# Kernel optimization log

Hardware: AMD Instinct MI355X
Metric: run time of the kernel (lower is better)

Reference implementation:

```python
import jax, jax.numpy as jnp
import numpy as np

P_MASK = 0.2
HALF = (2, 25, 25)            # n_consecutive // 2 for (T, H, W)
NPIX = 5 * 51 * 51            # np.prod(n_consecutive) = 13005


def setup_inputs() -> dict:
    key = jax.random.key(0)
    ks = jax.random.split(key, 10)
    B, T, H, W, C = 4, 32, 224, 224, 3
    N = 2000
    frames = jax.random.normal(ks[0], (B, T, H, W, C), dtype=jnp.float32)
    mask_token = jax.random.normal(ks[1], (C,), dtype=jnp.float32)
    b = jax.random.randint(ks[2], (N,), 0, B)
    t = jax.random.randint(ks[3], (N,), 0, T)
    h = jax.random.randint(ks[4], (N,), 0, H)
    w = jax.random.randint(ks[5], (N,), 0, W)
    rb = jax.random.randint(ks[6], (1,), 0, B)
    rt = jax.random.randint(ks[7], (1,), 0, T)
    rh = jax.random.randint(ks[8], (1,), 0, H)
    rw = jax.random.randint(ks[9], (1,), 0, W)
    return dict(frames=frames, mask_token=mask_token, b=b, t=t, h=h, w=w,
                rb=rb, rt=rt, rh=rh, rw=rw)


def _axis_mask(idx, half, size):
    # [n_box, size] float indicator of max(0, idx-half) <= pos < min(idx+half, size-1)
    lo = jnp.maximum(idx - half, 0)[:, None]
    hi = jnp.minimum(idx + half, size - 1)[:, None]   # torch slice upper bound uses size-1
    pos = jnp.arange(size)[None, :]
    return ((pos >= lo) & (pos < hi)).astype(jnp.float32)


def _box_union(b, t, h, w, B, T, H, W):
    # union of all boxes as a single rank-1-factor contraction (no per-box scatter)
    bi = (jnp.arange(B)[None, :] == b[:, None]).astype(jnp.float32)
    ti = _axis_mask(t, HALF[0], T)
    hi = _axis_mask(h, HALF[1], H)
    wi = _axis_mask(w, HALF[2], W)
    return jnp.einsum('ib,it,ih,iw->bthw', bi, ti, hi, wi) > 0


def reference(frames, mask_token, b, t, h, w, rb, rt, rh, rw):
    B, T, H, W, C = frames.shape
    tnpix = B * T * H * W
    n1 = int(tnpix * P_MASK * 0.8 // NPIX)
    n2 = int(tnpix * P_MASK * 0.1 // NPIX)
    R1 = _box_union(b[:n1], t[:n1], h[:n1], w[:n1], B, T, H, W)
    R2 = _box_union(b[n1:n1 + n2], t[n1:n1 + n2], h[n1:n1 + n2], w[n1:n1 + n2], B, T, H, W)
    R3 = _box_union(b[n1 + n2:n1 + 2 * n2], t[n1 + n2:n1 + 2 * n2],
                    h[n1 + n2:n1 + 2 * n2], w[n1 + n2:n1 + 2 * n2], B, T, H, W)
    random_token = frames[rb[0], rt[0], rh[0], rw[0]]   # [C]
    out = jnp.where(R1[..., None], mask_token, frames)
    out = jnp.where(R2[..., None], random_token, out)
    M = (R1 | R2 | R3).reshape(B, T, -1).any(axis=-1)
    return out, M
```

## Files before the change

### kernel.cpp

```cpp
#include <hip/hip_runtime.h>

namespace {
constexpr int B_ = 4, T_ = 32, H_ = 224, W_ = 224;
constexpr int HW_ = H_ * W_;
constexpr int NPIX_ = B_ * T_ * HW_;
constexpr int N1_ = 79;
constexpr int N2_ = 9;
constexpr int NBOX_RW_ = N1_ + N2_;
constexpr int NBOX_M_  = N1_ + 2 * N2_;
constexpr int HALF_T = 2, HALF_HW = 25;
}

__global__ __launch_bounds__(128) void build_slice_rects(
    const float* __restrict__ frames,
    const int* __restrict__ bb, const int* __restrict__ tt,
    const int* __restrict__ hh, const int* __restrict__ ww,
    const int* __restrict__ rb, const int* __restrict__ rt,
    const int* __restrict__ rh, const int* __restrict__ rw,
    int2* __restrict__ counts, int4* __restrict__ rects,
    float* __restrict__ rtok, float* __restrict__ Mout)
{
    __shared__ int lb[NBOX_M_], ltlo[NBOX_M_], lthi[NBOX_M_];
    __shared__ int4 lrect[NBOX_M_];

    int s = threadIdx.x;
    if (s == 0) {
        long idx = (((long)rb[0] * T_ + rt[0]) * H_ + rh[0]) * W_ + rw[0];
        rtok[0] = frames[idx * 3 + 0];
        rtok[1] = frames[idx * 3 + 1];
        rtok[2] = frames[idx * 3 + 2];
    }
    if (s < NBOX_M_) {
        lb[s]   = bb[s];
        ltlo[s] = max(tt[s] - HALF_T, 0);
        lthi[s] = min(tt[s] + HALF_T, T_ - 1);
        int4 r;
        r.x = max(hh[s] - HALF_HW, 0);
        r.y = min(hh[s] + HALF_HW, H_ - 1);
        r.z = max(ww[s] - HALF_HW, 0);
        r.w = min(ww[s] + HALF_HW, W_ - 1);
        lrect[s] = r;
    }
    __syncthreads();

    int sb = s / T_, st = s % T_;
    int c1 = 0, c2 = 0;
    bool any = false;
    int4* rs = rects + s * NBOX_RW_;
    for (int i = 0; i < NBOX_M_; ++i) {
        if (lb[i] != sb || st < ltlo[i] || st >= lthi[i]) continue;
        any = true;
        if (i >= NBOX_RW_) continue;
        if (i < N1_) rs[c1++] = lrect[i];
        else         rs[N1_ + c2++] = lrect[i];
    }
    counts[s] = make_int2(c1, c2);
    Mout[s] = any ? 1.0f : 0.0f;
}

__global__ __launch_bounds__(256) void apply_mask(
    const float* __restrict__ frames, const float* __restrict__ mtok,
    const int2* __restrict__ counts, const int4* __restrict__ rects,
    const float* __restrict__ rtok, float* __restrict__ out)
{
    int gid = blockIdx.x * blockDim.x + threadIdx.x;
    int p0 = gid * 8;

    const float4* fin = (const float4*)(frames + (long)p0 * 3);
    float4 f[6];
#pragma unroll
    for (int k = 0; k < 6; ++k) f[k] = fin[k];

    int s  = p0 / HW_;
    int hw = p0 - s * HW_;
    int h  = hw / W_;
    int w0 = hw - h * W_;

    int2 c = counts[s];
    const int4* rs = rects + s * NBOX_RW_;
    unsigned m1 = 0, m2 = 0;
    for (int j = 0; j < c.x; ++j) {
        int4 r = rs[j];
        if (h >= r.x && h < r.y) {
            int lo = max(r.z - w0, 0), hi = min(r.w - w0, 8);
            if (hi > lo) m1 |= ((1u << (hi - lo)) - 1u) << lo;
        }
    }
    for (int j = 0; j < c.y; ++j) {
        int4 r = rs[N1_ + j];
        if (h >= r.x && h < r.y) {
            int lo = max(r.z - w0, 0), hi = min(r.w - w0, 8);
            if (hi > lo) m2 |= ((1u << (hi - lo)) - 1u) << lo;
        }
    }

    if (m1 | m2) {
        float mt0 = mtok[0], mt1 = mtok[1], mt2 = mtok[2];
        float rt0 = rtok[0], rt1 = rtok[1], rt2 = rtok[2];
        float* v = (float*)f;
#pragma unroll
        for (int k = 0; k < 8; ++k) {
            bool b2 = (m2 >> k) & 1u, b1 = (m1 >> k) & 1u;
            v[k * 3 + 0] = b2 ? rt0 : (b1 ? mt0 : v[k * 3 + 0]);
            v[k * 3 + 1] = b2 ? rt1 : (b1 ? mt1 : v[k * 3 + 1]);
            v[k * 3 + 2] = b2 ? rt2 : (b1 ? mt2 : v[k * 3 + 2]);
        }
    }

    float4* fo = (float4*)(out + (long)p0 * 3);
#pragma unroll
    for (int k = 0; k < 6; ++k) fo[k] = f[k];
}

extern "C" void kernel_launch(void* const* d_in, const int* in_sizes, int n_in,
                              void* d_out, int out_size, void* d_ws, size_t ws_size,
                              hipStream_t stream)
{
    const float* frames = (const float*)d_in[0];
    const float* mtok   = (const float*)d_in[1];
    const int* b  = (const int*)d_in[2];
    const int* t  = (const int*)d_in[3];
    const int* h  = (const int*)d_in[4];
    const int* w  = (const int*)d_in[5];
    const int* rb = (const int*)d_in[6];
    const int* rt = (const int*)d_in[7];
    const int* rh = (const int*)d_in[8];
    const int* rw = (const int*)d_in[9];

    int2*  counts = (int2*)d_ws;
    int4*  rects  = (int4*)((char*)d_ws + 1024);
    float* rtok   = (float*)((char*)d_ws + 1024 + (size_t)128 * NBOX_RW_ * 16);

    float* out_frames = (float*)d_out;
    float* out_M      = out_frames + (long)NPIX_ * 3;

    build_slice_rects<<<1, 128, 0, stream>>>(frames, b, t, h, w, rb, rt, rh, rw,
                                             counts, rects, rtok, out_M);

    int nthreads = NPIX_ / 8;
    apply_mask<<<nthreads / 256, 256, 0, stream>>>(frames, mtok, counts, rects,
                                                   rtok, out_frames);
}
```

Before: 176.4 us.

## Precompute per-group bitmasks in parallel prepass and simplify apply kernel

The setup kernel now runs one block per (b,t) slice. It collects the relevant boxes through shared-memory atomics and writes a packed 16-pixel bitmask for every pixel group, holding the R1 bits in the low half and the R2 bits in the high half. The apply kernel then reads a single word per thread instead of looping over rectangles, and each thread handles 16 pixels rather than 8, with a launch-bounds occupancy hint. The aim is to take the per-pixel rectangle scanning out of the bandwidth-bound pass, at the cost of an extra mask buffer write/read and more registers per thread.

```diff
diff --git a/kernel.cpp b/kernel.cpp
--- a/kernel.cpp
+++ b/kernel.cpp
@@ -9,97 +9,102 @@
 constexpr int NBOX_RW_ = N1_ + N2_;
 constexpr int NBOX_M_  = N1_ + 2 * N2_;
 constexpr int HALF_T = 2, HALF_HW = 25;
+constexpr int GPT_ = 16;
+constexpr int GPR_ = W_ / GPT_;
+constexpr int GPS_ = H_ * GPR_;
+constexpr int NGRP_ = B_ * T_ * GPS_;
 }
 
-__global__ __launch_bounds__(128) void build_slice_rects(
+__global__ __launch_bounds__(256) void build_masks(
     const float* __restrict__ frames,
     const int* __restrict__ bb, const int* __restrict__ tt,
     const int* __restrict__ hh, const int* __restrict__ ww,
     const int* __restrict__ rb, const int* __restrict__ rt,
     const int* __restrict__ rh, const int* __restrict__ rw,
-    int2* __restrict__ counts, int4* __restrict__ rects,
-    float* __restrict__ rtok, float* __restrict__ Mout)
+    unsigned* __restrict__ gmask, float* __restrict__ rtok,
+    float* __restrict__ Mout)
 {
-    __shared__ int lb[NBOX_M_], ltlo[NBOX_M_], lthi[NBOX_M_];
-    __shared__ int4 lrect[NBOX_M_];
+    __shared__ int4 r1[NBOX_RW_];
+    __shared__ int4 r2[N2_];
+    __shared__ int c1, c2, c3;
+    const int s = blockIdx.x;
+    const int tid = threadIdx.x;
+    if (tid == 0) { c1 = 0; c2 = 0; c3 = 0; }
+    __syncthreads();
 
-    int s = threadIdx.x;
-    if (s == 0) {
+    if (s == 0 && tid == 0) {
         long idx = (((long)rb[0] * T_ + rt[0]) * H_ + rh[0]) * W_ + rw[0];
         rtok[0] = frames[idx * 3 + 0];
         rtok[1] = frames[idx * 3 + 1];
         rtok[2] = frames[idx * 3 + 2];
     }
-    if (s < NBOX_M_) {
-        lb[s]   = bb[s];
-        ltlo[s] = max(tt[s] - HALF_T, 0);
-        lthi[s] = min(tt[s] + HALF_T, T_ - 1);
-        int4 r;
-        r.x = max(hh[s] - HALF_HW, 0);
-        r.y = min(hh[s] + HALF_HW, H_ - 1);
-        r.z = max(ww[s] - HALF_HW, 0);
-        r.w = min(ww[s] + HALF_HW, W_ - 1);
-        lrect[s] = r;
+
+    const int sb = s / T_, st = s % T_;
+    if (tid < NBOX_M_) {
+        const int i = tid;
+        int tlo = max(tt[i] - HALF_T, 0);
+        int thi = min(tt[i] + HALF_T, T_ - 1);
+        if (bb[i] == sb && st >= tlo && st < thi) {
+            if (i >= NBOX_RW_) {
+                atomicAdd(&c3, 1);
+            } else {
+                int4 r;
+                r.x = max(hh[i] - HALF_HW, 0);
+                r.y = min(hh[i] + HALF_HW, H_ - 1);
+                r.z = max(ww[i] - HALF_HW, 0);
+                r.w = min(ww[i] + HALF_HW, W_ - 1);
+                if (i < N1_) r1[atomicAdd(&c1, 1)] = r;
+                else         r2[atomicAdd(&c2, 1)] = r;
+            }
+        }
     }
     __syncthreads();
 
-    int sb = s / T_, st = s % T_;
-    int c1 = 0, c2 = 0;
-    bool any = false;
-    int4* rs = rects + s * NBOX_RW_;
-    for (int i = 0; i < NBOX_M_; ++i) {
-        if (lb[i] != sb || st < ltlo[i] || st >= lthi[i]) continue;
-        any = true;
-        if (i >= NBOX_RW_) continue;
-        if (i < N1_) rs[c1++] = lrect[i];
-        else         rs[N1_ + c2++] = lrect[i];
+    if (tid == 0) Mout[s] = (c1 + c2 + c3) > 0 ? 1.0f : 0.0f;
+
+    const int n1 = c1, n2 = c2;
+    for (int g = tid; g < GPS_; g += 256) {
+        int h  = g / GPR_;
+        int w0 = (g - h * GPR_) * GPT_;
+        unsigned m1 = 0, m2 = 0;
+        for (int j = 0; j < n1; ++j) {
+            int4 r = r1[j];
+            if (h >= r.x && h < r.y) {
+                int lo = max(r.z - w0, 0), hi = min(r.w - w0, GPT_);
+                if (hi > lo) m1 |= ((1u << (hi - lo)) - 1u) << lo;
+            }
+        }
+        for (int j = 0; j < n2; ++j) {
+            int4 r = r2[j];
+            if (h >= r.x && h < r.y) {
+                int lo = max(r.z - w0, 0), hi = min(r.w - w0, GPT_);
+                if (hi > lo) m2 |= ((1u << (hi - lo)) - 1u) << lo;
+            }
+        }
+        gmask[s * GPS_ + g] = m1 | (m2 << 16);
     }
-    counts[s] = make_int2(c1, c2);
-    Mout[s] = any ? 1.0f : 0.0f;
 }
 
-__global__ __launch_bounds__(256) void apply_mask(
+__global__ __launch_bounds__(256, 4) void apply_mask(
     const float* __restrict__ frames, const float* __restrict__ mtok,
-    const int2* __restrict__ counts, const int4* __restrict__ rects,
-    const float* __restrict__ rtok, float* __restrict__ out)
+    const unsigned* __restrict__ gmask, const float* __restrict__ rtok,
+    float* __restrict__ out)
 {
-    int gid = blockIdx.x * blockDim.x + threadIdx.x;
-    int p0 = gid * 8;
+    const int gid = blockIdx.x * 256 + threadIdx.x;
+    const unsigned mw = gmask[gid];
 
-    const float4* fin = (const float4*)(frames + (long)p0 * 3);
-    float4 f[6];
+    const float4* fin = (const float4*)(frames + (long)gid * (GPT_ * 3));
+    float4 f[12];
 #pragma unroll
-    for (int k = 0; k < 6; ++k) f[k] = fin[k];
+    for (int k = 0; k < 12; ++k) f[k] = fin[k];
 
-    int s  = p0 / HW_;
-    int hw = p0 - s * HW_;
-    int h  = hw / W_;
-    int w0 = hw - h * W_;
-
-    int2 c = counts[s];
-    const int4* rs = rects + s * NBOX_RW_;
-    unsigned m1 = 0, m2 = 0;
-    for (int j = 0; j < c.x; ++j) {
-        int4 r = rs[j];
-        if (h >= r.x && h < r.y) {
-            int lo = max(r.z - w0, 0), hi = min(r.w - w0, 8);
-            if (hi > lo) m1 |= ((1u << (hi - lo)) - 1u) << lo;
-        }
-    }
-    for (int j = 0; j < c.y; ++j) {
-        int4 r = rs[N1_ + j];
-        if (h >= r.x && h < r.y) {
-            int lo = max(r.z - w0, 0), hi = min(r.w - w0, 8);
-            if (hi > lo) m2 |= ((1u << (hi - lo)) - 1u) << lo;
-        }
-    }
-
-    if (m1 | m2) {
+    if (mw) {
         float mt0 = mtok[0], mt1 = mtok[1], mt2 = mtok[2];
         float rt0 = rtok[0], rt1 = rtok[1], rt2 = rtok[2];
+        unsigned m1 = mw & 0xFFFFu, m2 = mw >> 16;
         float* v = (float*)f;
 #pragma unroll
-        for (int k = 0; k < 8; ++k) {
+        for (int k = 0; k < GPT_; ++k) {
             bool b2 = (m2 >> k) & 1u, b1 = (m1 >> k) & 1u;
             v[k * 3 + 0] = b2 ? rt0 : (b1 ? mt0 : v[k * 3 + 0]);
             v[k * 3 + 1] = b2 ? rt1 : (b1 ? mt1 : v[k * 3 + 1]);
@@ -107,9 +112,9 @@
         }
     }
 
-    float4* fo = (float4*)(out + (long)p0 * 3);
+    float4* fo = (float4*)(out + (long)gid * (GPT_ * 3));
 #pragma unroll
-    for (int k = 0; k < 6; ++k) fo[k] = f[k];
+    for (int k = 0; k < 12; ++k) fo[k] = f[k];
 }
 
 extern "C" void kernel_launch(void* const* d_in, const int* in_sizes, int n_in,
@@ -127,17 +132,15 @@
     const int* rh = (const int*)d_in[8];
     const int* rw = (const int*)d_in[9];
 
-    int2*  counts = (int2*)d_ws;
-    int4*  rects  = (int4*)((char*)d_ws + 1024);
-    float* rtok   = (float*)((char*)d_ws + 1024 + (size_t)128 * NBOX_RW_ * 16);
+    unsigned* gmask = (unsigned*)d_ws;
+    float*    rtok  = (float*)((char*)d_ws + (size_t)NGRP_ * 4);
 
     float* out_frames = (float*)d_out;
     float* out_M      = out_frames + (long)NPIX_ * 3;
 
-    build_slice_rects<<<1, 128, 0, stream>>>(frames, b, t, h, w, rb, rt, rh, rw,
-                                             counts, rects, rtok, out_M);
+    build_masks<<<B_ * T_, 256, 0, stream>>>(frames, b, t, h, w, rb, rt, rh, rw,
+                                             gmask, rtok, out_M);
 
-    int nthreads = NPIX_ / 8;
-    apply_mask<<<nthreads / 256, 256, 0, stream>>>(frames, mtok, counts, rects,
-                                                   rtok, out_frames);
+    apply_mask<<<NGRP_ / 256, 256, 0, stream>>>(frames, mtok, gmask, rtok,
+                                                out_frames);
 }
```

Result: slower. 183.7 us (+4.2%).
